# Kernel tuning notes

Hardware: AMD Instinct MI355X
Metric: run time of the kernel (lower is better)

The kernel has to match this reference:

```python
import jax, jax.numpy as jnp
import numpy as np

B, NQ, NK, H = 4, 2048, 2048, 512
TEMP = 1.0


def setup_inputs() -> dict:
    key = jax.random.key(0)
    ks = jax.random.split(key, 13)
    s = 0.02
    inp = {
        "query_feat": jax.random.normal(ks[0], (B, NQ, H), jnp.float32),
        "key_feat": jax.random.normal(ks[1], (B, NK, H), jnp.float32),
        "qm_uncert": jax.random.normal(ks[2], (B, NQ), jnp.float32),
        "md_uncert": jax.random.normal(ks[3], (B, NK), jnp.float32),
        "Wq": jax.random.normal(ks[4], (H, H), jnp.float32) * s,
        "bq": jnp.zeros((H,), jnp.float32),
        "Wk": jax.random.normal(ks[5], (H, H), jnp.float32) * s,
        "bk": jnp.zeros((H,), jnp.float32),
        "Wv": jax.random.normal(ks[6], (H, H), jnp.float32) * s,
        "bv": jnp.zeros((H,), jnp.float32),
        "Wo": jax.random.normal(ks[7], (H, H), jnp.float32) * s,
        "bo": jnp.zeros((H,), jnp.float32),
        "tau": jnp.float32(1.0),
    }
    return inp


def reference(query_feat, key_feat, qm_uncert, md_uncert,
              Wq, bq, Wk, bk, Wv, bv, Wo, bo, tau):
    h = query_feat.shape[-1]
    Q = query_feat @ Wq.T + bq          # [B,Nq,H]
    K = key_feat @ Wk.T + bk            # [B,Nk,H]
    V = key_feat @ Wv.T + bv            # [B,Nk,H]

    # scaled dot-product logits
    logits = jnp.einsum('bqh,bkh->bqk', Q, K) / jnp.sqrt(jnp.asarray(h, logits_dtype(Q)))

    # uncertainty weight: sigmoid(tau * (qm_i + md_j)), then sanitize (mult mode)
    u = jax.nn.sigmoid(tau * (qm_uncert[:, :, None] + md_uncert[:, None, :]))
    u = jnp.nan_to_num(u, nan=1.0, posinf=1e6, neginf=1e-6)
    u = jnp.clip(u, 1e-6, 1e6)
    row_sum = jnp.sum(jnp.abs(u), axis=-1, keepdims=True)
    u = jnp.where(row_sum <= 1e-12, jnp.asarray(1e-6, u.dtype), u)

    logits = (logits * u) / TEMP

    # rows fully masked to -1e9 get zeroed (no mask here, but kept for faithfulness)
    all_masked = jnp.all(logits == -1e9, axis=-1, keepdims=True)
    logits = jnp.where(all_masked, jnp.zeros_like(logits), logits)

    attn = jax.nn.softmax(logits, axis=-1)  # dropout p=0 -> identity
    att = jnp.einsum('bqk,bkh->bqh', attn, V)
    out = att @ Wo.T + bo
    return out, attn


def logits_dtype(x):
    return x.dtype
```

## Files before the change

kernel.cpp:

```cpp
#include <hip/hip_runtime.h>
#include <stdint.h>

#define DEVI static __device__ __forceinline__

typedef unsigned short u16;
typedef short bf16x8 __attribute__((ext_vector_type(8)));
typedef u16 u16x8 __attribute__((ext_vector_type(8)));
typedef u16 u16x4 __attribute__((ext_vector_type(4)));
typedef float f32x4 __attribute__((ext_vector_type(4)));

DEVI u16 f2bf(float f) {
    uint32_t u = __builtin_bit_cast(uint32_t, f);
    u += 0x7FFFu + ((u >> 16) & 1u);
    return (u16)(u >> 16);
}
DEVI float bf2f(u16 u) { return __builtin_bit_cast(float, (uint32_t)u << 16); }

struct GemmArgs {
    const void* A;
    const void* A2;
    long long aStrideBytes;
    int lda;
    const u16* Bm;
    long long bStrideElts;
    int ldb;
    int K;
    const float* bias; const float* bias2; const float* bias3;
    u16* outB;
    float* outF;
    long long outFStride;
    const float* qm; const float* md; const float* tauPtr; float scale;
    float* partials;
    const float* invsPtr;
    float* invsOut;
    u16* vt;
};

enum { EPI_PROJ3 = 0, EPI_LOGITS = 1, EPI_LOGITSB = 2, EPI_PV = 3, EPI_OUT = 4 };

template <int EPI, int AMODE, int TM>
__global__ __launch_bounds__(256, 4) void gemm_bt(GemmArgs p) {
    constexpr int NF = (TM == 128) ? 4 : 2;
    __shared__ u16 As[2][TM * 32];
    __shared__ u16 Bs[2][128 * 32];
    __shared__ float redBuf[2][128];
    __shared__ float sInvLds[128];

    const int tid = threadIdx.x;
    const int lane = tid & 63;
    const int wave = tid >> 6;
    const int g = lane >> 4, lr = lane & 15;
    const int waveRowBase = (TM == 128) ? (wave >> 1) * 64 : 0;
    const int waveColBase = (TM == 128) ? (wave & 1) * 64 : wave * 32;
    const int z = blockIdx.z;
    const int rowBase = blockIdx.x * TM;
    const int colBase = blockIdx.y * 128;

    int batch = z, koff = 0;
    if constexpr (EPI == EPI_PV) { batch = z & 3; koff = (z >> 2) * p.K; }

    const char* Abase;
    const float* bias = p.bias;
    const u16* Bbase;
    if constexpr (EPI == EPI_PROJ3) {
        Abase = (const char*)(z == 0 ? p.A : p.A2);
        Bbase = p.Bm + (size_t)z * 512 * 512;
        bias = (z == 0) ? p.bias : (z == 1 ? p.bias2 : p.bias3);
    } else {
        Abase = (const char*)p.A + (size_t)batch * p.aStrideBytes + (size_t)koff * (AMODE == 1 ? 4 : 2);
        Bbase = p.Bm + (size_t)batch * p.bStrideElts + koff;
    }

    if constexpr (EPI == EPI_PV && AMODE == 0) {
        if (blockIdx.y == 4) {
            if (tid < 128) {
                const float* pp = p.partials + ((size_t)batch * 2048 + rowBase + tid) * 16;
                float s = 0.f;
                #pragma unroll
                for (int t = 0; t < 16; ++t) s += pp[t];
                float inv = 1.0f / s;
                sInvLds[tid] = inv;
                p.invsOut[batch * 2048 + rowBase + tid] = inv;
            }
            __syncthreads();
            const u16* e = (const u16*)Abase + (size_t)rowBase * 2048;
            float* attnOut = p.outF + (size_t)batch * p.outFStride + (size_t)rowBase * 2048 + koff;
            #pragma unroll 4
            for (int it = 0; it < 64; ++it) {
                int cc = it * 256 + tid;
                int row = cc >> 7, colc = (cc & 127) * 8;
                float s = sInvLds[row];
                u16x8 v = *(const u16x8*)(e + (size_t)row * 2048 + colc);
                f32x4 f0, f1;
                f0[0] = bf2f(v[0]) * s; f0[1] = bf2f(v[1]) * s;
                f0[2] = bf2f(v[2]) * s; f0[3] = bf2f(v[3]) * s;
                f1[0] = bf2f(v[4]) * s; f1[1] = bf2f(v[5]) * s;
                f1[2] = bf2f(v[6]) * s; f1[3] = bf2f(v[7]) * s;
                float* dst = attnOut + (size_t)row * 2048 + colc;
                __builtin_nontemporal_store(f0, (f32x4*)dst);
                __builtin_nontemporal_store(f1, (f32x4*)dst + 1);
            }
            return;
        }
    }

    f32x4 acc[4][NF] = {};

    const int nk = p.K >> 5;

    if constexpr (AMODE == 0) {
        auto stage = [&](int buf, int kt) {
            const int kb = kt << 5;
            #pragma unroll
            for (int i = 0; i < TM / 64; ++i) {
                int c = i * 256 + tid;
                const u16* gp = (const u16*)Abase + (size_t)(rowBase + (c >> 2)) * p.lda + kb + (c & 3) * 8;
                char* lp = (char*)&As[buf][0] + (i * 256 + wave * 64) * 16;
                __builtin_amdgcn_global_load_lds((const __attribute__((address_space(1))) void*)gp,
                                                 (__attribute__((address_space(3))) void*)lp, 16, 0, 0);
            }
            #pragma unroll
            for (int i = 0; i < 2; ++i) {
                int c = i * 256 + tid;
                const u16* gp = Bbase + (size_t)(colBase + (c >> 2)) * p.ldb + kb + (c & 3) * 8;
                char* lp = (char*)&Bs[buf][0] + (i * 256 + wave * 64) * 16;
                __builtin_amdgcn_global_load_lds((const __attribute__((address_space(1))) void*)gp,
                                                 (__attribute__((address_space(3))) void*)lp, 16, 0, 0);
            }
        };
        stage(0, 0);
        asm volatile("s_waitcnt vmcnt(0)" ::: "memory");
        __builtin_amdgcn_s_barrier();
        for (int kt = 0; kt < nk; ++kt) {
            const int cur = kt & 1;
            if (kt + 1 < nk) stage(cur ^ 1, kt + 1);
            bf16x8 af[4], bfr[NF];
            #pragma unroll
            for (int m = 0; m < 4; ++m)
                af[m] = *(const bf16x8*)&As[cur][(waveRowBase + m * 16 + lr) * 32 + g * 8];
            #pragma unroll
            for (int n = 0; n < NF; ++n)
                bfr[n] = *(const bf16x8*)&Bs[cur][(waveColBase + n * 16 + lr) * 32 + g * 8];
            __builtin_amdgcn_s_setprio(1);
            #pragma unroll
            for (int m = 0; m < 4; ++m)
                #pragma unroll
                for (int n = 0; n < NF; ++n)
                    acc[m][n] = __builtin_amdgcn_mfma_f32_16x16x32_bf16(af[m], bfr[n], acc[m][n], 0, 0, 0);
            __builtin_amdgcn_s_setprio(0);
            asm volatile("s_waitcnt vmcnt(0)" ::: "memory");
            __builtin_amdgcn_s_barrier();
        }
    } else {
        const int arow2 = tid >> 2, kh2 = (tid & 3) << 3;
        const u16* pa0 = nullptr; const u16* pa1 = nullptr; float sInv = 1.0f;
        if constexpr (AMODE == 2) {
            pa0 = (const u16*)p.A + (size_t)(rowBase + arow2) * 512 + kh2;
            pa1 = pa0 + (size_t)8192 * 512;
            sInv = p.invsPtr ? p.invsPtr[rowBase + arow2] : 1.0f;
        }
        for (int kt = 0; kt < nk; ++kt) {
            const int kb = kt << 5;
            float4 areg[4]; u16x8 a0, a1;
            if constexpr (AMODE == 1) {
                const float* Af = (const float*)Abase;
                const int arow = tid >> 1, kh = (tid & 1) << 4;
                const float* src = Af + (size_t)(rowBase + arow) * p.lda + kb + kh;
                #pragma unroll
                for (int j = 0; j < 4; ++j) areg[j] = ((const float4*)src)[j];
            } else {
                a0 = *(const u16x8*)(pa0 + kb);
                a1 = *(const u16x8*)(pa1 + kb);
            }
            __syncthreads();
            if constexpr (AMODE == 1) {
                const int arow = tid >> 1, kh = (tid & 1) << 4;
                u16 tmp[16];
                #pragma unroll
                for (int j = 0; j < 4; ++j) {
                    tmp[4 * j + 0] = f2bf(areg[j].x);
                    tmp[4 * j + 1] = f2bf(areg[j].y);
                    tmp[4 * j + 2] = f2bf(areg[j].z);
                    tmp[4 * j + 3] = f2bf(areg[j].w);
                }
                #pragma unroll
                for (int h = 0; h < 2; ++h)
                    *(u16x8*)&As[0][arow * 32 + kh + h * 8] = *(u16x8*)&tmp[h * 8];
            } else {
                u16 tmp[8];
                #pragma unroll
                for (int j = 0; j < 8; ++j)
                    tmp[j] = f2bf((bf2f(a0[j]) + bf2f(a1[j])) * sInv);
                *(u16x8*)&As[0][arow2 * 32 + kh2] = *(u16x8*)tmp;
            }
            #pragma unroll
            for (int i = 0; i < 2; ++i) {
                int c = i * 256 + tid;
                const u16* gp = Bbase + (size_t)(colBase + (c >> 2)) * p.ldb + kb + (c & 3) * 8;
                char* lp = (char*)&Bs[0][0] + (i * 256 + wave * 64) * 16;
                __builtin_amdgcn_global_load_lds((const __attribute__((address_space(1))) void*)gp,
                                                 (__attribute__((address_space(3))) void*)lp, 16, 0, 0);
            }
            __syncthreads();

            bf16x8 af[4], bfr[NF];
            #pragma unroll
            for (int m = 0; m < 4; ++m)
                af[m] = *(const bf16x8*)&As[0][(waveRowBase + m * 16 + lr) * 32 + g * 8];
            #pragma unroll
            for (int n = 0; n < NF; ++n)
                bfr[n] = *(const bf16x8*)&Bs[0][(waveColBase + n * 16 + lr) * 32 + g * 8];
            #pragma unroll
            for (int m = 0; m < 4; ++m)
                #pragma unroll
                for (int n = 0; n < NF; ++n)
                    acc[m][n] = __builtin_amdgcn_mfma_f32_16x16x32_bf16(af[m], bfr[n], acc[m][n], 0, 0, 0);
        }
    }

    const int rB = rowBase + waveRowBase;
    const int cB = colBase + waveColBase;

    if constexpr (EPI == EPI_PROJ3) {
        if (z < 2) {
            u16* dst = p.outB + (size_t)z * 8192 * 512;
            #pragma unroll
            for (int n = 0; n < NF; ++n) {
                int col = cB + n * 16 + lr;
                float bv = bias[col];
                #pragma unroll
                for (int m = 0; m < 4; ++m) {
                    int r0 = rB + m * 16 + g * 4;
                    #pragma unroll
                    for (int i = 0; i < 4; ++i)
                        dst[(size_t)(r0 + i) * 512 + col] = f2bf(acc[m][n][i] + bv);
                }
            }
        } else {
            #pragma unroll
            for (int n = 0; n < NF; ++n) {
                int col = cB + n * 16 + lr;
                float bv = bias[col];
                #pragma unroll
                for (int m = 0; m < 4; ++m) {
                    int r0 = rB + m * 16 + g * 4;
                    int b = r0 >> 11, k0 = r0 & 2047;
                    u16x4 pk;
                    #pragma unroll
                    for (int i = 0; i < 4; ++i) pk[i] = f2bf(acc[m][n][i] + bv);
                    *(u16x4*)&p.vt[((size_t)b * 512 + col) * 2048 + k0] = pk;
                }
            }
        }
    } else if constexpr (EPI == EPI_LOGITS || EPI == EPI_LOGITSB) {
        const float* qmB = p.qm + z * 2048;
        const float* mdB = p.md + z * 2048;
        const float tau = *p.tauPtr;
        float* outRow = p.outF + (size_t)z * p.outFStride;
        float mdv[NF];
        #pragma unroll
        for (int n = 0; n < NF; ++n) mdv[n] = mdB[cB + n * 16 + lr];
        #pragma unroll
        for (int m = 0; m < 4; ++m) {
            int r0 = rB + m * 16 + g * 4;
            #pragma unroll
            for (int i = 0; i < 4; ++i) {
                int q = r0 + i;
                float qv = qmB[q];
                float rs = 0.f;
                #pragma unroll
                for (int n = 0; n < NF; ++n) {
                    float t = tau * (qv + mdv[n]);
                    float u = 1.0f / (1.0f + __expf(-t));
                    u = fminf(fmaxf(u, 1e-6f), 1e6f);
                    float e = __expf(acc[m][n][i] * p.scale * u);
                    if (EPI == EPI_LOGITSB)
                        p.outB[((size_t)(z * 2048 + q)) * 2048 + cB + n * 16 + lr] = f2bf(e);
                    else
                        outRow[(size_t)q * 2048 + cB + n * 16 + lr] = e;
                    rs += e;
                }
                #pragma unroll
                for (int off = 1; off < 16; off <<= 1) rs += __shfl_xor(rs, off, 64);
                if (lr == 0) redBuf[wave & 1][waveRowBase + m * 16 + g * 4 + i] = rs;
            }
        }
        __syncthreads();
        if (tid < 128) {
            float s = redBuf[0][tid] + redBuf[1][tid];
            int q = rowBase + tid;
            p.partials[((size_t)z * 2048 + q) * 16 + blockIdx.y] = s;
        }
    } else if constexpr (EPI == EPI_PV) {
        const int split = z >> 2;
        u16* dst = p.outB + (size_t)split * 8192 * 512;
        #pragma unroll
        for (int n = 0; n < NF; ++n) {
            int col = cB + n * 16 + lr;
            #pragma unroll
            for (int m = 0; m < 4; ++m) {
                int r0 = rB + m * 16 + g * 4;
                size_t gr = (size_t)batch * 2048 + r0;
                #pragma unroll
                for (int i = 0; i < 4; ++i)
                    dst[(gr + i) * 512 + col] = f2bf(acc[m][n][i]);
            }
        }
    } else {
        #pragma unroll
        for (int n = 0; n < NF; ++n) {
            int col = cB + n * 16 + lr;
            float bv = p.bias[col];
            #pragma unroll
            for (int m = 0; m < 4; ++m) {
                int r0 = rB + m * 16 + g * 4;
                #pragma unroll
                for (int i = 0; i < 4; ++i)
                    __builtin_nontemporal_store(acc[m][n][i] + bv, &p.outF[(size_t)(r0 + i) * 512 + col]);
            }
        }
    }
}

__global__ void cvt_all2(const float* Wq, const float* Wk, const float* Wv, const float* Wo,
                         const float* qf, const float* kf,
                         u16* wdst, u16* qdst, u16* kdst) {
    const size_t WSZ = (size_t)512 * 512;
    const size_t FSZ = (size_t)8192 * 512;
    size_t i = ((size_t)blockIdx.x * 256 + threadIdx.x) * 4;
    const float* src; u16* dstp;
    if (i < 4 * WSZ) {
        int w = (int)(i / WSZ);
        src = (w == 0 ? Wq : w == 1 ? Wk : w == 2 ? Wv : Wo) + (i - (size_t)w * WSZ);
        dstp = wdst + i;
    } else if (i < 4 * WSZ + FSZ) {
        size_t off = i - 4 * WSZ;
        src = qf + off; dstp = qdst + off;
    } else {
        size_t off = i - 4 * WSZ - FSZ;
        src = kf + off; dstp = kdst + off;
    }
    float4 v = *(const float4*)src;
    u16x4 u = { f2bf(v.x), f2bf(v.y), f2bf(v.z), f2bf(v.w) };
    *(u16x4*)dstp = u;
}

__global__ void rowsum_inv(const float* __restrict__ partials, float* __restrict__ invs) {
    int r = blockIdx.x * 256 + threadIdx.x;
    float s = 0.f;
    #pragma unroll
    for (int t = 0; t < 16; ++t) s += partials[r * 16 + t];
    invs[r] = 1.0f / s;
}

__global__ void normalize_attn(float* __restrict__ attn, const float* __restrict__ invs) {
    size_t i4 = (size_t)blockIdx.x * 256 + threadIdx.x;
    int row = (int)(i4 >> 9);
    float s = invs[row];
    float4 v = ((const float4*)attn)[i4];
    v.x *= s; v.y *= s; v.z *= s; v.w *= s;
    ((float4*)attn)[i4] = v;
}

extern "C" void kernel_launch(void* const* d_in, const int* in_sizes, int n_in,
                              void* d_out, int out_size, void* d_ws, size_t ws_size,
                              hipStream_t stream) {
    const float* qf  = (const float*)d_in[0];
    const float* kf  = (const float*)d_in[1];
    const float* qm  = (const float*)d_in[2];
    const float* md  = (const float*)d_in[3];
    const float* Wq  = (const float*)d_in[4];
    const float* bq  = (const float*)d_in[5];
    const float* Wk  = (const float*)d_in[6];
    const float* bk  = (const float*)d_in[7];
    const float* Wv  = (const float*)d_in[8];
    const float* bv  = (const float*)d_in[9];
    const float* Wo  = (const float*)d_in[10];
    const float* bo  = (const float*)d_in[11];
    const float* tau = (const float*)d_in[12];

    float* out  = (float*)d_out;
    float* attn = out + (size_t)4 * 2048 * 512;

    const size_t NV = (size_t)8192 * 512;
    u16* Qb   = (u16*)d_ws;
    u16* Kb   = Qb + NV;
    u16* Vtb  = Kb + NV;
    u16* Wqb  = Vtb + NV;
    u16* Wob  = Wqb + (size_t)3 * 512 * 512;
    float* partials = (float*)(Wqb + (size_t)4 * 512 * 512);
    float* invs = partials + (size_t)8192 * 16;
    u16* attE = (u16*)(invs + 8192);
    u16* qfB  = attE + (size_t)4 * 2048 * 2048;
    u16* kfB  = qfB + NV;
    size_t need = (size_t)((char*)(kfB + NV) - (char*)d_ws);
    const bool big = ws_size >= need;

    u16* partialPV = Qb;

    dim3 blk(256);

    GemmArgs a = {};
    a.lda = 512; a.ldb = 512; a.K = 512;
    a.bias = bq; a.bias2 = bk; a.bias3 = bv;
    a.outB = Qb; a.vt = Vtb;
    if (big) {
        cvt_all2<<<dim3(9216), blk, 0, stream>>>(Wq, Wk, Wv, Wo, qf, kf, Wqb, qfB, kfB);
        a.A = qfB; a.A2 = kfB; a.Bm = Wqb;
        gemm_bt<EPI_PROJ3, 0, 128><<<dim3(64, 4, 3), blk, 0, stream>>>(a);
    } else {
        cvt_all2<<<dim3(1024), blk, 0, stream>>>(Wq, Wk, Wv, Wo, qf, kf, Wqb, nullptr, nullptr);
        a.A = qf; a.A2 = kf; a.Bm = Wqb;
        gemm_bt<EPI_PROJ3, 1, 128><<<dim3(64, 4, 3), blk, 0, stream>>>(a);
    }

    GemmArgs lg = {};
    lg.A = Qb; lg.aStrideBytes = (long long)2048 * 512 * 2; lg.lda = 512;
    lg.Bm = Kb; lg.bStrideElts = (long long)2048 * 512; lg.ldb = 512;
    lg.K = 512;
    lg.qm = qm; lg.md = md; lg.tauPtr = tau;
    lg.scale = 0.04419417382415922f;
    lg.partials = partials;
    if (big) {
        lg.outB = attE;
        gemm_bt<EPI_LOGITSB, 0, 128><<<dim3(16, 16, 4), blk, 0, stream>>>(lg);
    } else {
        lg.outF = attn; lg.outFStride = (long long)2048 * 2048;
        gemm_bt<EPI_LOGITS, 0, 128><<<dim3(16, 16, 4), blk, 0, stream>>>(lg);
    }

    GemmArgs pv = {};
    pv.Bm = Vtb; pv.bStrideElts = (long long)512 * 2048; pv.ldb = 2048;
    pv.K = 1024; pv.outB = partialPV; pv.lda = 2048;
    pv.partials = partials; pv.invsOut = invs;
    if (big) {
        pv.A = attE; pv.aStrideBytes = (long long)2048 * 2048 * 2;
        pv.outF = attn; pv.outFStride = (long long)2048 * 2048;
        gemm_bt<EPI_PV, 0, 128><<<dim3(16, 5, 8), blk, 0, stream>>>(pv);
    } else {
        rowsum_inv<<<dim3(32), blk, 0, stream>>>(partials, invs);
        normalize_attn<<<dim3(16384), blk, 0, stream>>>(attn, invs);
        pv.A = attn; pv.aStrideBytes = (long long)2048 * 2048 * 4;
        gemm_bt<EPI_PV, 1, 128><<<dim3(16, 4, 8), blk, 0, stream>>>(pv);
    }

    GemmArgs og = {};
    og.A = partialPV; og.lda = 512;
    og.Bm = Wob; og.ldb = 512;
    og.K = 512; og.bias = bo; og.outF = out;
    og.invsPtr = big ? invs : nullptr;
    gemm_bt<EPI_OUT, 2, 64><<<dim3(128, 4, 1), blk, 0, stream>>>(og);
}
```

Before: 128.2 us.

## Triple-buffer GEMM loads, remap blocks across XCDs, precompute sigmoid exponentials

```diff
diff --git a/kernel.cpp b/kernel.cpp
--- a/kernel.cpp
+++ b/kernel.cpp
@@ -15,6 +15,17 @@
     return (u16)(u >> 16);
 }
 DEVI float bf2f(u16 u) { return __builtin_bit_cast(float, (uint32_t)u << 16); }
+
+DEVI void xcd_remap(int& bx, int& by, int& bz, bool yfast) {
+    int nx = gridDim.x, ny = gridDim.y, nz = gridDim.z;
+    int nwg = nx * ny * nz;
+    if (nwg & 7) return;
+    int f = yfast ? (by + ny * (bx + nx * bz))
+                  : (bx + nx * (by + ny * bz));
+    int fp = (f >> 3) + (nwg >> 3) * (f & 7);
+    if (yfast) { by = fp % ny; bx = (fp / ny) % nx; bz = fp / (ny * nx); }
+    else       { bx = fp % nx; by = (fp / nx) % ny; bz = fp / (nx * ny); }
+}
 
 struct GemmArgs {
     const void* A;
@@ -39,10 +50,11 @@
 enum { EPI_PROJ3 = 0, EPI_LOGITS = 1, EPI_LOGITSB = 2, EPI_PV = 3, EPI_OUT = 4 };
 
 template <int EPI, int AMODE, int TM>
-__global__ __launch_bounds__(256, 4) void gemm_bt(GemmArgs p) {
+__global__ __launch_bounds__(256, AMODE == 0 ? 3 : 4) void gemm_bt(GemmArgs p) {
+    constexpr int NBUF = (AMODE == 0) ? 3 : 1;
     constexpr int NF = (TM == 128) ? 4 : 2;
-    __shared__ u16 As[2][TM * 32];
-    __shared__ u16 Bs[2][128 * 32];
+    __shared__ u16 As[NBUF][TM * 32];
+    __shared__ u16 Bs[NBUF][128 * 32];
     __shared__ float redBuf[2][128];
     __shared__ float sInvLds[128];
 
@@ -52,9 +64,12 @@
     const int g = lane >> 4, lr = lane & 15;
     const int waveRowBase = (TM == 128) ? (wave >> 1) * 64 : 0;
     const int waveColBase = (TM == 128) ? (wave & 1) * 64 : wave * 32;
-    const int z = blockIdx.z;
-    const int rowBase = blockIdx.x * TM;
-    const int colBase = blockIdx.y * 128;
+
+    int bxR = blockIdx.x, byR = blockIdx.y, bzR = blockIdx.z;
+    xcd_remap(bxR, byR, bzR, EPI == EPI_OUT);
+    const int z = bzR;
+    const int rowBase = bxR * TM;
+    const int colBase = byR * 128;
 
     int batch = z, koff = 0;
     if constexpr (EPI == EPI_PV) { batch = z & 3; koff = (z >> 2) * p.K; }
@@ -72,7 +87,7 @@
     }
 
     if constexpr (EPI == EPI_PV && AMODE == 0) {
-        if (blockIdx.y == 4) {
+        if (byR == 4) {
             if (tid < 128) {
                 const float* pp = p.partials + ((size_t)batch * 2048 + rowBase + tid) * 16;
                 float s = 0.f;
@@ -129,11 +144,15 @@
             }
         };
         stage(0, 0);
-        asm volatile("s_waitcnt vmcnt(0)" ::: "memory");
+        stage(1, 1);
+        asm volatile("s_waitcnt vmcnt(4)" ::: "memory");
         __builtin_amdgcn_s_barrier();
+        int cur = 0;
         for (int kt = 0; kt < nk; ++kt) {
-            const int cur = kt & 1;
-            if (kt + 1 < nk) stage(cur ^ 1, kt + 1);
+            if (kt + 2 < nk) {
+                int sbuf = (cur == 0) ? 2 : cur - 1;
+                stage(sbuf, kt + 2);
+            }
             bf16x8 af[4], bfr[NF];
             #pragma unroll
             for (int m = 0; m < 4; ++m)
@@ -148,8 +167,12 @@
                 for (int n = 0; n < NF; ++n)
                     acc[m][n] = __builtin_amdgcn_mfma_f32_16x16x32_bf16(af[m], bfr[n], acc[m][n], 0, 0, 0);
             __builtin_amdgcn_s_setprio(0);
-            asm volatile("s_waitcnt vmcnt(0)" ::: "memory");
+            if (kt + 2 < nk)
+                asm volatile("s_waitcnt vmcnt(4)" ::: "memory");
+            else
+                asm volatile("s_waitcnt vmcnt(0)" ::: "memory");
             __builtin_amdgcn_s_barrier();
+            cur = (cur == 2) ? 0 : cur + 1;
         }
     } else {
         const int arow2 = tid >> 2, kh2 = (tid & 3) << 3;
@@ -253,27 +276,25 @@
             }
         }
     } else if constexpr (EPI == EPI_LOGITS || EPI == EPI_LOGITSB) {
-        const float* qmB = p.qm + z * 2048;
-        const float* mdB = p.md + z * 2048;
-        const float tau = *p.tauPtr;
+        const float* eqB = p.qm + z * 2048;
+        const float* emB = p.md + z * 2048;
         float* outRow = p.outF + (size_t)z * p.outFStride;
-        float mdv[NF];
+        float emv[NF];
         #pragma unroll
-        for (int n = 0; n < NF; ++n) mdv[n] = mdB[cB + n * 16 + lr];
+        for (int n = 0; n < NF; ++n) emv[n] = emB[cB + n * 16 + lr];
         #pragma unroll
         for (int m = 0; m < 4; ++m) {
             int r0 = rB + m * 16 + g * 4;
             #pragma unroll
             for (int i = 0; i < 4; ++i) {
                 int q = r0 + i;
-                float qv = qmB[q];
+                float eqv = eqB[q];
                 float rs = 0.f;
                 #pragma unroll
                 for (int n = 0; n < NF; ++n) {
-                    float t = tau * (qv + mdv[n]);
-                    float u = 1.0f / (1.0f + __expf(-t));
-                    u = fminf(fmaxf(u, 1e-6f), 1e6f);
-                    float e = __expf(acc[m][n][i] * p.scale * u);
+                    float u = 1.0f / (1.0f + eqv * emv[n]);
+                    u = fmaxf(u, 1e-6f);
+                    float e = exp2f(acc[m][n][i] * p.scale * u);
                     if (EPI == EPI_LOGITSB)
                         p.outB[((size_t)(z * 2048 + q)) * 2048 + cB + n * 16 + lr] = f2bf(e);
                     else
@@ -289,7 +310,7 @@
         if (tid < 128) {
             float s = redBuf[0][tid] + redBuf[1][tid];
             int q = rowBase + tid;
-            p.partials[((size_t)z * 2048 + q) * 16 + blockIdx.y] = s;
+            p.partials[((size_t)z * 2048 + q) * 16 + byR] = s;
         }
     } else if constexpr (EPI == EPI_PV) {
         const int split = z >> 2;
@@ -322,9 +343,18 @@
     }
 }
 
-__global__ void cvt_all2(const float* Wq, const float* Wk, const float* Wv, const float* Wo,
+__global__ void cvt_all3(const float* Wq, const float* Wk, const float* Wv, const float* Wo,
                          const float* qf, const float* kf,
-                         u16* wdst, u16* qdst, u16* kdst) {
+                         const float* qm, const float* md, const float* tauPtr,
+                         u16* wdst, u16* qdst, u16* kdst,
+                         float* eq, float* em) {
+    if (blockIdx.x >= gridDim.x - 64) {
+        int j = (blockIdx.x - (gridDim.x - 64)) * 256 + threadIdx.x;
+        float tau = *tauPtr;
+        if (j < 8192) eq[j] = __expf(-tau * qm[j]);
+        else          em[j - 8192] = __expf(-tau * md[j - 8192]);
+        return;
+    }
     const size_t WSZ = (size_t)512 * 512;
     const size_t FSZ = (size_t)8192 * 512;
     size_t i = ((size_t)blockIdx.x * 256 + threadIdx.x) * 4;
@@ -390,7 +420,9 @@
     u16* Wob  = Wqb + (size_t)3 * 512 * 512;
     float* partials = (float*)(Wqb + (size_t)4 * 512 * 512);
     float* invs = partials + (size_t)8192 * 16;
-    u16* attE = (u16*)(invs + 8192);
+    float* eq = invs + 8192;
+    float* em = eq + 8192;
+    u16* attE = (u16*)(em + 8192);
     u16* qfB  = attE + (size_t)4 * 2048 * 2048;
     u16* kfB  = qfB + NV;
     size_t need = (size_t)((char*)(kfB + NV) - (char*)d_ws);
@@ -405,11 +437,13 @@
     a.bias = bq; a.bias2 = bk; a.bias3 = bv;
     a.outB = Qb; a.vt = Vtb;
     if (big) {
-        cvt_all2<<<dim3(9216), blk, 0, stream>>>(Wq, Wk, Wv, Wo, qf, kf, Wqb, qfB, kfB);
+        cvt_all3<<<dim3(9280), blk, 0, stream>>>(Wq, Wk, Wv, Wo, qf, kf, qm, md, tau,
+                                                 Wqb, qfB, kfB, eq, em);
         a.A = qfB; a.A2 = kfB; a.Bm = Wqb;
         gemm_bt<EPI_PROJ3, 0, 128><<<dim3(64, 4, 3), blk, 0, stream>>>(a);
     } else {
-        cvt_all2<<<dim3(1024), blk, 0, stream>>>(Wq, Wk, Wv, Wo, qf, kf, Wqb, nullptr, nullptr);
+        cvt_all3<<<dim3(1088), blk, 0, stream>>>(Wq, Wk, Wv, Wo, qf, kf, qm, md, tau,
+                                                 Wqb, nullptr, nullptr, eq, em);
         a.A = qf; a.A2 = kf; a.Bm = Wqb;
         gemm_bt<EPI_PROJ3, 1, 128><<<dim3(64, 4, 3), blk, 0, stream>>>(a);
     }
@@ -418,8 +452,8 @@
     lg.A = Qb; lg.aStrideBytes = (long long)2048 * 512 * 2; lg.lda = 512;
     lg.Bm = Kb; lg.bStrideElts = (long long)2048 * 512; lg.ldb = 512;
     lg.K = 512;
-    lg.qm = qm; lg.md = md; lg.tauPtr = tau;
-    lg.scale = 0.04419417382415922f;
+    lg.qm = eq; lg.md = em; lg.tauPtr = tau;
+    lg.scale = 0.04419417382415922f * 1.4426950408889634f;
     lg.partials = partials;
     if (big) {
         lg.outB = attE;
```

Result: slower. 133.3 us (+4.0%).
